# Kernel optimization log

Hardware: AMD Instinct MI355X
Metric: run time of the kernel (lower is better)

## Reference

```python
import jax, jax.numpy as jnp
import numpy as np

NUM_HEADS = 8
NEG_SLOPE = 0.2


def setup_inputs() -> dict:
    key = jax.random.key(0)
    k1, k2, k3, k4 = jax.random.split(key, 4)
    B, N, D_IN, D_K, D_V = 4, 4096, 256, 256, 256
    x = jax.random.normal(k1, (B, N, D_IN), dtype=jnp.float32)
    Wq = jax.random.normal(k2, (D_IN, D_K), dtype=jnp.float32) * (1.0 / np.sqrt(D_IN))
    Wk = jax.random.normal(k3, (D_IN, D_K), dtype=jnp.float32) * (1.0 / np.sqrt(D_IN))
    Wv = jax.random.normal(k4, (D_IN, D_V), dtype=jnp.float32) * (1.0 / np.sqrt(D_IN))
    return {"x": x, "Wq": Wq, "Wk": Wk, "Wv": Wv}


def reference(x, Wq, Wk, Wv):
    B, N, _ = x.shape
    nh = NUM_HEADS
    dim_k = Wq.shape[1]
    dim_v = Wv.shape[1]
    dk, dv = dim_k // nh, dim_v // nh
    nor_fact = 1.0 / np.sqrt(dk)
    # project and split heads: [B, H, N, dk]
    q = (x @ Wq).reshape(B, N, nh, dk).transpose(0, 2, 1, 3)
    k = (x @ Wk).reshape(B, N, nh, dk).transpose(0, 2, 1, 3)
    v = (x @ Wv).reshape(B, N, nh, dv).transpose(0, 2, 1, 3)
    # all-pairs scores, scaled then LeakyReLU (no softmax)
    dist = jnp.einsum('bhnd,bhmd->bhnm', q, k) * nor_fact
    dist = jnp.where(dist >= 0, dist, NEG_SLOPE * dist)
    att = jnp.einsum('bhnm,bhmd->bhnd', dist, v)
    return att.transpose(0, 2, 1, 3).reshape(B, N, dim_v)
```

## Files before the change

### kernel.cpp

```cpp
#include <hip/hip_runtime.h>

typedef __attribute__((ext_vector_type(8))) short short8;
typedef __attribute__((ext_vector_type(4))) float f32x4;
typedef __attribute__((ext_vector_type(2))) unsigned int u32x2;
typedef __attribute__((ext_vector_type(4))) unsigned int u32x4;

#define MFMA16x32(A, B, C) \
  __builtin_amdgcn_mfma_f32_16x16x32_bf16((A), (B), (C), 0, 0, 0)

__device__ __forceinline__ void async_cp16(const unsigned short* g, void* l) {
  __builtin_amdgcn_global_load_lds(
      (const __attribute__((address_space(1))) unsigned int*)g,
      (__attribute__((address_space(3))) unsigned int*)l, 16, 0, 0);
}

__device__ __forceinline__ unsigned int fbits(float f) {
  return __builtin_bit_cast(unsigned int, f);
}
__device__ __forceinline__ unsigned int pack_bf16(float a, float b) {
  return __builtin_amdgcn_perm(fbits(b), fbits(a), 0x07060302u);
}
__device__ __forceinline__ unsigned short bf16_rne(float f) {
  unsigned int u = fbits(f);
  return (unsigned short)((u + 0x8000u) >> 16);
}

__global__ __launch_bounds__(256) void prep_kernel(
    const float* __restrict__ x, unsigned short* __restrict__ xb,
    const float* __restrict__ Wq, const float* __restrict__ Wk,
    const float* __restrict__ Wv, unsigned short* __restrict__ WT) {
  __shared__ float tile[32][33];
  if (blockIdx.x < 4096) {
    const size_t i = ((size_t)blockIdx.x * 256 + threadIdx.x) * 4;
    const float4 f = *(const float4*)(x + i);
    u32x2 u = {(unsigned int)bf16_rne(f.x) | ((unsigned int)bf16_rne(f.y) << 16),
               (unsigned int)bf16_rne(f.z) | ((unsigned int)bf16_rne(f.w) << 16)};
    *(u32x2*)(xb + i) = u;
    return;
  }
  const int bid = blockIdx.x - 4096;
  const int g = bid / 64, rem = bid % 64;
  const int k0 = (rem >> 3) * 32, n0 = (rem & 7) * 32;
  const float* W = (g == 0) ? Wq : (g == 1) ? Wk : Wv;
  const int t = threadIdx.x;
  {
    const int kr = t >> 3, nc = (t & 7) * 4;
    const float4 f = *(const float4*)(W + (size_t)(k0 + kr) * 256 + n0 + nc);
    tile[kr][nc + 0] = f.x; tile[kr][nc + 1] = f.y;
    tile[kr][nc + 2] = f.z; tile[kr][nc + 3] = f.w;
  }
  __syncthreads();
  {
    const int nr = t >> 3, kc = (t & 7) * 4;
    unsigned int u0 = (unsigned int)bf16_rne(tile[kc + 0][nr]) |
                      ((unsigned int)bf16_rne(tile[kc + 1][nr]) << 16);
    unsigned int u1 = (unsigned int)bf16_rne(tile[kc + 2][nr]) |
                      ((unsigned int)bf16_rne(tile[kc + 3][nr]) << 16);
    u32x2 u = {u0, u1};
    *(u32x2*)(WT + (size_t)g * 65536 + (size_t)(n0 + nr) * 256 + k0 + kc) = u;
  }
}

__global__ __launch_bounds__(256, 2) void proj_kernel(
    const unsigned short* __restrict__ xb, const unsigned short* __restrict__ WT,
    unsigned short* __restrict__ QH, unsigned short* __restrict__ KH,
    unsigned short* __restrict__ VT) {
  __shared__ __align__(16) char smem[65536];
  const int tid = threadIdx.x;
  const int w = tid >> 6, lane = tid & 63, l15 = lane & 15, quad = lane >> 4;
  const int bid = blockIdx.x;
  const int mtile = bid / 6, nt = bid % 6;
  const int g = nt >> 1, n0 = (nt & 1) * 128;
  const int m0 = mtile * 128;

  const int srow = lane >> 3, useg = lane & 7;
  const int swz = (useg ^ srow) * 8;
  const unsigned short* aS = xb + (size_t)(m0 + w * 32 + srow) * 256 + swz;
  const unsigned short* bS =
      WT + (size_t)g * 65536 + (size_t)(n0 + w * 32 + srow) * 256 + swz;

#pragma unroll
  for (int j = 0; j < 4; j++) {
    async_cp16(aS + j * 2048, smem + w * 4096 + j * 1024);
    async_cp16(bS + j * 2048, smem + 16384 + w * 4096 + j * 1024);
  }
  __syncthreads();

  const f32x4 zero = {0.f, 0.f, 0.f, 0.f};
  f32x4 acc[2][8];
#pragma unroll
  for (int s = 0; s < 2; s++)
#pragma unroll
    for (int c = 0; c < 8; c++) acc[s][c] = zero;

  const int sw = l15 & 7;
  for (int t = 0; t < 4; t++) {
    const int nb = t & 1;
    const int kn = ((t + 1) & 3) * 64;
#pragma unroll
    for (int j = 0; j < 4; j++) {
      async_cp16(aS + kn + j * 2048,
                 smem + (nb ^ 1) * 32768 + w * 4096 + j * 1024);
      async_cp16(bS + kn + j * 2048,
                 smem + (nb ^ 1) * 32768 + 16384 + w * 4096 + j * 1024);
    }
    const char* Ab = smem + nb * 32768;
    const char* Bb = Ab + 16384;
#pragma unroll
    for (int ks = 0; ks < 2; ks++) {
      const int seg = ((ks * 4 + quad) ^ sw) * 16;
      short8 af[2], bf[8];
#pragma unroll
      for (int s = 0; s < 2; s++)
        af[s] = *(const short8*)(Ab + (w * 32 + s * 16 + l15) * 128 + seg);
#pragma unroll
      for (int c = 0; c < 8; c++)
        bf[c] = *(const short8*)(Bb + (c * 16 + l15) * 128 + seg);
      if (g < 2) {
#pragma unroll
        for (int s = 0; s < 2; s++)
#pragma unroll
          for (int c = 0; c < 8; c++)
            acc[s][c] = MFMA16x32(bf[c], af[s], acc[s][c]);
      } else {
#pragma unroll
        for (int s = 0; s < 2; s++)
#pragma unroll
          for (int c = 0; c < 8; c++)
            acc[s][c] = MFMA16x32(af[s], bf[c], acc[s][c]);
      }
    }
    __syncthreads();
  }

  if (g < 2) {
    unsigned short* O = g ? KH : QH;
    const float sc = g ? 1.0f : 0.17677669529663688f;
#pragma unroll
    for (int s = 0; s < 2; s++)
#pragma unroll
      for (int c = 0; c < 8; c++) {
        const int row = m0 + w * 32 + s * 16 + l15;
        const int col = n0 + c * 16 + quad * 4;
        const int bb = row >> 12, nn = row & 4095;
        const int hh = col >> 5, dl = col & 31;
        u32x2 pk = {pack_bf16(acc[s][c][0] * sc, acc[s][c][1] * sc),
                    pack_bf16(acc[s][c][2] * sc, acc[s][c][3] * sc)};
        *(u32x2*)(O + ((size_t)(bb * 8 + hh) * 4096 + nn) * 32 + dl) = pk;
      }
  } else {
#pragma unroll
    for (int s = 0; s < 2; s++)
#pragma unroll
      for (int c = 0; c < 8; c++) {
        const int col = n0 + c * 16 + l15;
        const int hh = col >> 5, dl = col & 31;
        const int row = m0 + w * 32 + s * 16 + quad * 4;
        const int bb = row >> 12;
        const int nn = (row & 4064) | (quad << 3) | ((s & 1) << 2);
        u32x2 pk = {pack_bf16(acc[s][c][0], acc[s][c][1]),
                    pack_bf16(acc[s][c][2], acc[s][c][3])};
        *(u32x2*)(VT + (size_t)((bb * 8 + hh) * 32 + dl) * 4096 + nn) = pk;
      }
  }
}

__global__ __launch_bounds__(512, 2) void attn_kernel(
    const unsigned short* __restrict__ QH, const unsigned short* __restrict__ KH,
    const unsigned short* __restrict__ VT, float* __restrict__ out) {
  __shared__ __align__(16) char smem[16384];
  const int tid = threadIdx.x;
  const int w = tid >> 6, lane = tid & 63, l15 = lane & 15, quad = lane >> 4;
  const int bid = blockIdx.x;
  const int bh = bid & 31, qh = bid >> 5;
  const int b = bh >> 3, h = bh & 7;
  const int qbase = qh * 512 + w * 64;

  const unsigned short* Qp =
      QH + ((size_t)bh * 4096 + qbase + l15) * 32 + quad * 8;
  short8 qf[4];
#pragma unroll
  for (int s = 0; s < 4; s++) qf[s] = *(const short8*)(Qp + (size_t)s * 512);

  const bool isK = (w < 4);
  const unsigned short* src0;
  int kstr, wbOff;
  if (isK) {
    const int key = w * 16 + (lane >> 2);
    const int gseg = (lane & 3) ^ ((lane >> 3) & 3);
    src0 = KH + ((size_t)bh * 4096 + key) * 32 + gseg * 8;
    kstr = 32;
    wbOff = w * 1024;
  } else {
    const int r = (w - 4) * 8 + (lane >> 3), useg = lane & 7;
    src0 = VT + ((size_t)bh * 32 + r) * 4096 + ((useg ^ (r & 7)) * 8);
    kstr = 1;
    wbOff = 4096 + (w - 4) * 1024;
  }

  async_cp16(src0, smem + wbOff);
  __syncthreads();

  const f32x4 zero = {0.f, 0.f, 0.f, 0.f};
  f32x4 acc[4][2];
#pragma unroll
  for (int s = 0; s < 4; s++) {
    acc[s][0] = zero;
    acc[s][1] = zero;
  }

  const int rs = l15 & 7;
  const int kseg = (quad ^ ((l15 >> 1) & 3)) * 16;
  for (int i = 0; i < 64; i++) {
    const int nb = i & 1;
    const int kn = ((i + 1) & 63) * 64;
    async_cp16(src0 + (size_t)kn * kstr, smem + (nb ^ 1) * 8192 + wbOff);

    const char* Kb = smem + nb * 8192;
    const char* Vb = Kb + 4096;
    short8 kf[4];
#pragma unroll
    for (int c = 0; c < 4; c++)
      kf[c] = *(const short8*)(Kb + (c * 16 + l15) * 64 + kseg);
    short8 vf[2][2];
#pragma unroll
    for (int dt = 0; dt < 2; dt++) {
      const char* Vr = Vb + (dt * 16 + l15) * 128;
#pragma unroll
      for (int u = 0; u < 2; u++)
        vf[dt][u] = *(const short8*)(Vr + (((4 * u + quad) ^ rs) * 16));
    }

#pragma unroll
    for (int s = 0; s < 4; s++) {
      unsigned int pp[4][2];
#pragma unroll
      for (int c = 0; c < 4; c++) {
        f32x4 st = MFMA16x32(kf[c], qf[s], zero);
        float t0 = fmaxf(st[0], 0.2f * st[0]);
        float t1 = fmaxf(st[1], 0.2f * st[1]);
        float t2 = fmaxf(st[2], 0.2f * st[2]);
        float t3 = fmaxf(st[3], 0.2f * st[3]);
        pp[c][0] = pack_bf16(t0, t1);
        pp[c][1] = pack_bf16(t2, t3);
      }
#pragma unroll
      for (int u = 0; u < 2; u++) {
        u32x4 bw = {pp[2 * u][0], pp[2 * u][1],
                    pp[2 * u + 1][0], pp[2 * u + 1][1]};
        short8 pb = __builtin_bit_cast(short8, bw);
#pragma unroll
        for (int dt = 0; dt < 2; dt++)
          acc[s][dt] = MFMA16x32(vf[dt][u], pb, acc[s][dt]);
      }
    }
    __syncthreads();
  }

#pragma unroll
  for (int s = 0; s < 4; s++)
#pragma unroll
    for (int dt = 0; dt < 2; dt++)
      *(f32x4*)(out + ((size_t)b * 4096 + qbase + s * 16 + l15) * 256 + h * 32 +
                dt * 16 + quad * 4) = acc[s][dt];
}

extern "C" void kernel_launch(void* const* d_in, const int* in_sizes, int n_in,
                              void* d_out, int out_size, void* d_ws,
                              size_t ws_size, hipStream_t stream) {
  const float* x = (const float*)d_in[0];
  const float* Wq = (const float*)d_in[1];
  const float* Wk = (const float*)d_in[2];
  const float* Wv = (const float*)d_in[3];
  float* out = (float*)d_out;

  unsigned short* ws = (unsigned short*)d_ws;
  unsigned short* QHb = ws;
  unsigned short* KHb = ws + 4194304;
  unsigned short* VTb = ws + 2 * 4194304;
  unsigned short* xbb = ws + 3 * 4194304;
  unsigned short* WTb = ws + 4 * 4194304;

  prep_kernel<<<4288, 256, 0, stream>>>(x, xbb, Wq, Wk, Wv, WTb);
  proj_kernel<<<768, 256, 0, stream>>>(xbb, WTb, QHb, KHb, VTb);
  attn_kernel<<<256, 512, 0, stream>>>(QHb, KHb, VTb, out);
}
```

Baseline: 172.6 us.

## Split key tiles across wave halves and reduce partial outputs via LDS

The attention kernel now assigns each of the 8 waves one of 4 query strips and one of 2 key halves per 64-key tile. This halves query rows per block and doubles the grid to 512 blocks. At the end, the two key-half partial accumulators are summed through shared memory before the store. The goal is to fill more CUs and raise occupancy (launch bounds 512,4). The cost is a larger LDS footprint and an extra reduction/sync step, and the packed LeakyReLU is done with a 2-wide vector max.

```diff
diff --git a/kernel.cpp b/kernel.cpp
--- a/kernel.cpp
+++ b/kernel.cpp
@@ -2,6 +2,7 @@
 
 typedef __attribute__((ext_vector_type(8))) short short8;
 typedef __attribute__((ext_vector_type(4))) float f32x4;
+typedef __attribute__((ext_vector_type(2))) float f32x2;
 typedef __attribute__((ext_vector_type(2))) unsigned int u32x2;
 typedef __attribute__((ext_vector_type(4))) unsigned int u32x4;
 
@@ -23,6 +24,12 @@
 __device__ __forceinline__ unsigned short bf16_rne(float f) {
   unsigned int u = fbits(f);
   return (unsigned short)((u + 0x8000u) >> 16);
+}
+__device__ __forceinline__ unsigned int leaky_pack(float a, float b) {
+  f32x2 v = {a, b};
+  f32x2 m = v * 0.2f;
+  f32x2 r = __builtin_elementwise_max(v, m);
+  return pack_bf16(r[0], r[1]);
 }
 
 __global__ __launch_bounds__(256) void prep_kernel(
@@ -165,16 +172,17 @@
   }
 }
 
-__global__ __launch_bounds__(512, 2) void attn_kernel(
+__global__ __launch_bounds__(512, 4) void attn_kernel(
     const unsigned short* __restrict__ QH, const unsigned short* __restrict__ KH,
     const unsigned short* __restrict__ VT, float* __restrict__ out) {
-  __shared__ __align__(16) char smem[16384];
+  __shared__ __align__(16) char smem[32768];
   const int tid = threadIdx.x;
   const int w = tid >> 6, lane = tid & 63, l15 = lane & 15, quad = lane >> 4;
   const int bid = blockIdx.x;
   const int bh = bid & 31, qh = bid >> 5;
   const int b = bh >> 3, h = bh & 7;
-  const int qbase = qh * 512 + w * 64;
+  const int khalf = w >> 2, strip = w & 3;
+  const int qbase = qh * 256 + strip * 64;
 
   const unsigned short* Qp =
       QH + ((size_t)bh * 4096 + qbase + l15) * 32 + quad * 8;
@@ -211,6 +219,7 @@
 
   const int rs = l15 & 7;
   const int kseg = (quad ^ ((l15 >> 1) & 3)) * 16;
+  const int voff = ((khalf * 4 + quad) ^ rs) * 16;
   for (int i = 0; i < 64; i++) {
     const int nb = i & 1;
     const int kn = ((i + 1) & 63) * 64;
@@ -218,51 +227,53 @@
 
     const char* Kb = smem + nb * 8192;
     const char* Vb = Kb + 4096;
-    short8 kf[4];
-#pragma unroll
-    for (int c = 0; c < 4; c++)
-      kf[c] = *(const short8*)(Kb + (c * 16 + l15) * 64 + kseg);
-    short8 vf[2][2];
-#pragma unroll
-    for (int dt = 0; dt < 2; dt++) {
-      const char* Vr = Vb + (dt * 16 + l15) * 128;
-#pragma unroll
-      for (int u = 0; u < 2; u++)
-        vf[dt][u] = *(const short8*)(Vr + (((4 * u + quad) ^ rs) * 16));
-    }
+    short8 kf[2];
+#pragma unroll
+    for (int c = 0; c < 2; c++)
+      kf[c] = *(const short8*)(Kb + ((khalf * 32 + c * 16 + l15) * 64) + kseg);
+    short8 vf[2];
+#pragma unroll
+    for (int dt = 0; dt < 2; dt++)
+      vf[dt] = *(const short8*)(Vb + (dt * 16 + l15) * 128 + voff);
 
 #pragma unroll
     for (int s = 0; s < 4; s++) {
-      unsigned int pp[4][2];
-#pragma unroll
-      for (int c = 0; c < 4; c++) {
+      u32x4 bw;
+#pragma unroll
+      for (int c = 0; c < 2; c++) {
         f32x4 st = MFMA16x32(kf[c], qf[s], zero);
-        float t0 = fmaxf(st[0], 0.2f * st[0]);
-        float t1 = fmaxf(st[1], 0.2f * st[1]);
-        float t2 = fmaxf(st[2], 0.2f * st[2]);
-        float t3 = fmaxf(st[3], 0.2f * st[3]);
-        pp[c][0] = pack_bf16(t0, t1);
-        pp[c][1] = pack_bf16(t2, t3);
-      }
-#pragma unroll
-      for (int u = 0; u < 2; u++) {
-        u32x4 bw = {pp[2 * u][0], pp[2 * u][1],
-                    pp[2 * u + 1][0], pp[2 * u + 1][1]};
-        short8 pb = __builtin_bit_cast(short8, bw);
-#pragma unroll
-        for (int dt = 0; dt < 2; dt++)
-          acc[s][dt] = MFMA16x32(vf[dt][u], pb, acc[s][dt]);
-      }
+        bw[2 * c] = leaky_pack(st[0], st[1]);
+        bw[2 * c + 1] = leaky_pack(st[2], st[3]);
+      }
+      short8 pb = __builtin_bit_cast(short8, bw);
+#pragma unroll
+      for (int dt = 0; dt < 2; dt++)
+        acc[s][dt] = MFMA16x32(vf[dt], pb, acc[s][dt]);
     }
     __syncthreads();
   }
 
-#pragma unroll
-  for (int s = 0; s < 4; s++)
-#pragma unroll
-    for (int dt = 0; dt < 2; dt++)
-      *(f32x4*)(out + ((size_t)b * 4096 + qbase + s * 16 + l15) * 256 + h * 32 +
-                dt * 16 + quad * 4) = acc[s][dt];
+  if (khalf) {
+    char* dst = smem + strip * 8192 + lane * 16;
+#pragma unroll
+    for (int s = 0; s < 4; s++)
+#pragma unroll
+      for (int dt = 0; dt < 2; dt++)
+        *(f32x4*)(dst + (s * 2 + dt) * 1024) = acc[s][dt];
+  }
+  __syncthreads();
+  if (!khalf) {
+    const char* srcp = smem + strip * 8192 + lane * 16;
+#pragma unroll
+    for (int s = 0; s < 4; s++)
+#pragma unroll
+      for (int dt = 0; dt < 2; dt++) {
+        f32x4 o = *(const f32x4*)(srcp + (s * 2 + dt) * 1024);
+        o += acc[s][dt];
+        *(f32x4*)(out + ((size_t)b * 4096 + qbase + s * 16 + l15) * 256 +
+                  h * 32 + dt * 16 + quad * 4) = o;
+      }
+  }
 }
 
 extern "C" void kernel_launch(void* const* d_in, const int* in_sizes, int n_in,
@@ -283,5 +294,5 @@
 
   prep_kernel<<<4288, 256, 0, stream>>>(x, xbb, Wq, Wk, Wv, WTb);
   proj_kernel<<<768, 256, 0, stream>>>(xbb, WTb, QHb, KHb, VTb);
-  attn_kernel<<<256, 512, 0, stream>>>(QHb, KHb, VTb, out);
-}
+  attn_kernel<<<512, 512, 0, stream>>>(QHb, KHb, VTb, out);
+}
```

New measurement: 173.5 us. Within noise of the previous version (+0.5%).
